# Optimization experiments

Measured on AMD Instinct MI355X. Metric: run time of the kernel, lower is better.

The kernel has to match this reference:

```python
import jax, jax.numpy as jnp
import numpy as np
from itertools import permutations

NEG = -1e30  # finite 'log-zero' sentinel to keep grads NaN-free
DEN_SCALE = 1.0


def fsm_log_marginal(llh, seqlen, src, dst, pdf, weight, init, final):
    """Log-marginal (total log path weight) of an FSM over a sequence.

    llh: [T, C] frame pdf log-likelihoods; arcs (src,dst,pdf,weight): [A];
    init/final: [N] state log-weights. Forward recursion:
      alpha_{t+1}[j] = logsumexp_{arcs a: dst=j} alpha_t[src_a] + w_a + llh[t, pdf_a]
    Frames t >= seqlen are identity (alpha frozen).
    """
    N = init.shape[0]
    T = llh.shape[0]

    def step(alpha, xs):
        llh_t, t = xs
        score = alpha[src] + weight + llh_t[pdf]  # [A]
        m = jnp.maximum(jax.ops.segment_max(score, dst, num_segments=N), NEG)
        s = jax.ops.segment_sum(jnp.exp(score - m[dst]), dst, num_segments=N)
        new = m + jnp.log(jnp.maximum(s, 1e-30))
        alpha = jnp.where(t < seqlen, new, alpha)
        return alpha, None

    alpha, _ = jax.lax.scan(step, init, (llh, jnp.arange(T)))
    return jax.nn.logsumexp(alpha + final)


# vmap over batch (FSM shared -> None axes) for the denominator
_den_b = jax.vmap(fsm_log_marginal, in_axes=(0, 0, None, None, None, None, None, None))
_den_sb = jax.vmap(_den_b, in_axes=(0, 0, None, None, None, None, None, None))
# vmap over (speaker, batch) with per-(s,b) numerator FSMs
_num_sb = jax.vmap(jax.vmap(fsm_log_marginal))


def reference(est_llhs, seqlengths, den_src, den_dst, den_pdf, den_weight,
              den_init, den_final, num_src, num_dst, num_pdf, num_weight,
              num_init, num_final):
    S = est_llhs.shape[1]
    llhs = jnp.transpose(est_llhs, (1, 0, 2, 3))  # [S, B, T, C]
    seql = seqlengths.T                           # [S, B]

    # denominator: shared graph, summed over speakers -> [B]
    den = _den_sb(llhs, seql, den_src, den_dst, den_pdf, den_weight,
                  den_init, den_final)  # [S, B]
    den_llh = den.sum(axis=0)

    # numerator: evaluate every speaker permutation, take min over perms
    num_per_perm = []
    for p in permutations(range(S)):
        pidx = jnp.array(p)
        nl = _num_sb(llhs[pidx], seql[pidx], num_src, num_dst, num_pdf,
                     num_weight, num_init, num_final)  # [S, B]
        num_per_perm.append(nl.sum(axis=0))
    num_llh = jnp.min(jnp.stack(num_per_perm, axis=1), axis=1)  # [B]

    loss = -(num_llh - DEN_SCALE * den_llh)
    return loss.sum()


def setup_inputs() -> dict:
    key = jax.random.key(0)
    ks = jax.random.split(key, 14)
    B, S, T, C = 8, 2, 512, 2048
    Nd, Ad = 1024, 16384   # denominator graph
    Nn, An = 256, 2048     # numerator graphs (per speaker, per utt)

    est_llhs = jax.nn.log_softmax(
        jax.random.normal(ks[0], (B, S, T, C), jnp.float32), axis=-1)
    seqlengths = jax.random.randint(ks[1], (B, S), T // 2, T + 1, jnp.int32)

    den_src = jax.random.randint(ks[2], (Ad,), 0, Nd, jnp.int32)
    den_dst = jax.random.randint(ks[3], (Ad,), 0, Nd, jnp.int32)
    den_pdf = jax.random.randint(ks[4], (Ad,), 0, C, jnp.int32)
    den_weight = 0.1 * jax.random.normal(ks[5], (Ad,), jnp.float32)
    den_init = jax.nn.log_softmax(jax.random.normal(ks[6], (Nd,), jnp.float32))
    den_final = jax.nn.log_softmax(jax.random.normal(ks[7], (Nd,), jnp.float32))

    num_src = jax.random.randint(ks[8], (S, B, An), 0, Nn, jnp.int32)
    num_dst = jax.random.randint(ks[9], (S, B, An), 0, Nn, jnp.int32)
    num_pdf = jax.random.randint(ks[10], (S, B, An), 0, C, jnp.int32)
    num_weight = 0.1 * jax.random.normal(ks[11], (S, B, An), jnp.float32)
    num_init = jax.nn.log_softmax(
        jax.random.normal(ks[12], (S, B, Nn), jnp.float32), axis=-1)
    num_final = jax.nn.log_softmax(
        jax.random.normal(ks[13], (S, B, Nn), jnp.float32), axis=-1)

    return {
        'est_llhs': est_llhs, 'seqlengths': seqlengths,
        'den_src': den_src, 'den_dst': den_dst, 'den_pdf': den_pdf,
        'den_weight': den_weight, 'den_init': den_init, 'den_final': den_final,
        'num_src': num_src, 'num_dst': num_dst, 'num_pdf': num_pdf,
        'num_weight': num_weight, 'num_init': num_init, 'num_final': num_final,
    }
```

## Files before the change

kernel.cpp:

```cpp
#include <hip/hip_runtime.h>
#include <cstdint>
#include <cstddef>

#define BB 8
#define SS 2
#define TT 512
#define CC 2048
#define ND 1024
#define AD 16384
#define NN 256
#define AN 2048
#define NEGV -1e30f
#define NTH 1024
#define NWG 256

__global__ void prep_kernel(const int* __restrict__ src, const int* __restrict__ dst,
                            const int* __restrict__ pdf, const float* __restrict__ w,
                            unsigned* __restrict__ meta_t, unsigned* __restrict__ pxi,
                            float* __restrict__ wcsr,
                            int* __restrict__ pbeg, int* __restrict__ padj,
                            int N, int A, int LC)
{
    __shared__ int cnt[1024];
    __shared__ int pos[1024];
    __shared__ unsigned char gcnt[8192];
    const int g = blockIdx.x;
    src += (size_t)g * A; dst += (size_t)g * A; pdf += (size_t)g * A; w += (size_t)g * A;
    meta_t += (size_t)g * A; pxi += (size_t)g * A; wcsr += (size_t)g * A;
    pbeg += (size_t)g * (N + 1); padj += (size_t)g * N;
    const int tid = threadIdx.x;
    cnt[tid] = 0;
    __syncthreads();
    for (int a = tid; a < A; a += blockDim.x) atomicAdd(&cnt[dst[a]], 1);
    __syncthreads();
    const int deg = cnt[tid];
    pos[tid] = deg;
    __syncthreads();
    for (int off = 1; off < blockDim.x; off <<= 1) {
        int add = (tid >= off) ? pos[tid - off] : 0;
        __syncthreads();
        pos[tid] += add;
        __syncthreads();
    }
    const int r0 = pos[tid] - deg;
    const int np = deg ? (((r0 + deg - 1) >> LC) - (r0 >> LC) + 1) : 0;
    __syncthreads();
    pos[tid] = np;
    __syncthreads();
    for (int off = 1; off < blockDim.x; off <<= 1) {
        int add = (tid >= off) ? pos[tid - off] : 0;
        __syncthreads();
        pos[tid] += add;
        __syncthreads();
    }
    const int pexcl = pos[tid] - np;
    pbeg[tid] = pexcl;
    if (tid == blockDim.x - 1) pbeg[N] = pexcl + np;
    padj[tid] = pexcl - (r0 >> LC);
    cnt[tid] = r0;
    __syncthreads();
    for (int a = tid; a < A; a += blockDim.x) {
        const int d2 = dst[a];
        const int p = atomicAdd(&cnt[d2], 1);
        const int l = p >> LC;
        const int i = p & ((1 << LC) - 1);
        meta_t[(size_t)i * NTH + l] = (unsigned)src[a] | ((unsigned)d2 << 16);
        pxi[p] = (unsigned)pdf[a];
        wcsr[p] = w[a];
    }
    __syncthreads();
    const int CH = 1 << LC;
    const int ngrp = (NTH / 64) * CH;
    if (tid < ngrp) {
        unsigned char* cb = &gcnt[tid * 32];
        for (int b = 0; b < 32; ++b) cb[b] = 0;
        const int i = tid & (CH - 1);
        const int w2 = tid >> LC;
        for (int lane = 0; lane < 64; ++lane) {
            const size_t idx = (size_t)i * NTH + (w2 * 64 + lane);
            const unsigned mt = meta_t[idx];
            const unsigned sv = mt & 0xffffu;
            const unsigned alt = sv ^ ((sv >> 5) & 31u);
            const int b0 = (int)(sv & 31u), b1 = (int)(alt & 31u);
            unsigned gx;
            if (cb[b1] < cb[b0]) { cb[b1]++; gx = (unsigned)N + alt; }
            else                 { cb[b0]++; gx = sv; }
            meta_t[idx] = (mt & 0xffff0000u) | gx;
        }
    }
}

__device__ void wprep_part(int ub, int nb, int t0, int Tt, const float* __restrict__ est,
                           const unsigned* __restrict__ pxi_den,
                           const float* __restrict__ wcsr_den,
                           const unsigned* __restrict__ pxi_num,
                           const float* __restrict__ wcsr_num,
                           float* __restrict__ Wd, float* __restrict__ Wn,
                           float* row_s)
{
    const int tid = threadIdx.x;
    const int nden = 16 * Tt;
    const int total = nden + 32 * Tt;
    for (int u = ub; u < total; u += nb) {
        __syncthreads();
        const float* row; const unsigned* pxi; const float* wcs; float* out; int n4;
        if (u < nden) {
            const int inst = u / Tt, trel = u - inst * Tt;
            const int s = inst >> 3, b = inst & 7;
            row = est + ((size_t)(b * SS + s) * TT + (t0 + trel)) * CC;
            pxi = pxi_den; wcs = wcsr_den;
            out = Wd + ((size_t)inst * Tt + trel) * AD;
            n4 = AD >> 2;
        } else {
            const int v = u - nden;
            const int inst = v / Tt, trel = v - inst * Tt;
            const int gg = inst & 15, p = inst >> 4;
            const int s = gg >> 3, b = gg & 7;
            const int sp = p ? (1 - s) : s;
            row = est + ((size_t)(b * SS + sp) * TT + (t0 + trel)) * CC;
            pxi = pxi_num + (size_t)gg * AN; wcs = wcsr_num + (size_t)gg * AN;
            out = Wn + ((size_t)inst * Tt + trel) * AN;
            n4 = AN >> 2;
        }
        row_s[tid] = row[tid]; row_s[tid + 1024] = row[tid + 1024];
        __syncthreads();
        const uint4* p4 = (const uint4*)pxi;
        const float4* w4 = (const float4*)wcs;
        float4* o4 = (float4*)out;
        for (int k = tid; k < n4; k += 1024) {
            const uint4 pp = p4[k];
            const float4 ww = w4[k];
            o4[k] = make_float4(row_s[pp.x] + ww.x, row_s[pp.y] + ww.y,
                                row_s[pp.z] + ww.z, row_s[pp.w] + ww.w);
        }
    }
}

__global__ __launch_bounds__(1024) void wprep0_kernel(
    const float* __restrict__ est,
    const unsigned* __restrict__ pxi_den, const float* __restrict__ wcsr_den,
    const unsigned* __restrict__ pxi_num, const float* __restrict__ wcsr_num,
    float* __restrict__ Wd, float* __restrict__ Wn, int t0, int Tt)
{
    __shared__ float row_s[CC];
    wprep_part(blockIdx.x, gridDim.x, t0, Tt, est, pxi_den, wcsr_den,
               pxi_num, wcsr_num, Wd, Wn, row_s);
}

template<int CH>
__device__ inline void load_w_row(const float* __restrict__ p, float* dst)
{
    if constexpr (CH == 16) {
        const float4* p4 = (const float4*)p;
        const float4 a = p4[0], b = p4[1], c = p4[2], d = p4[3];
        dst[0]=a.x;  dst[1]=a.y;  dst[2]=a.z;  dst[3]=a.w;
        dst[4]=b.x;  dst[5]=b.y;  dst[6]=b.z;  dst[7]=b.w;
        dst[8]=c.x;  dst[9]=c.y;  dst[10]=c.z; dst[11]=c.w;
        dst[12]=d.x; dst[13]=d.y; dst[14]=d.z; dst[15]=d.w;
    } else {
        const float2 v = *(const float2*)p;
        dst[0] = v.x; dst[1] = v.y;
    }
}

template<int CH>
__device__ void fsm_forward_tile(int N, int L, int t0, int Tt, bool first, bool last,
    const float* __restrict__ Wrow0, int wstride,
    const unsigned* __restrict__ meta_g,
    const int* __restrict__ pbeg_g, const int* __restrict__ padj_g,
    const float* __restrict__ initv, const float* __restrict__ finalv,
    float* __restrict__ alpha_gl, float* __restrict__ res,
    float* alpha_s, float2* pk)
{
    const int tid = threadIdx.x;
    unsigned meta[CH];
#pragma unroll
    for (int i = 0; i < CH; ++i) meta[i] = meta_g[i * NTH + tid];
    unsigned segmask = 0;
#pragma unroll
    for (int i = 0; i < CH; ++i) {
        const int di = (int)(meta[i] >> 16);
        const int dn = (i + 1 < CH) ? (int)(meta[i + 1] >> 16) : -1;
        if (di != dn) segmask |= (1u << i);
    }
    const int slot0 = padj_g[meta[0] >> 16] + tid;
    const bool st = tid < N;
    int pb0 = 0, pb1 = 0; float fin = 0.f;
    if (st) {
        const float a0 = first ? initv[tid] : alpha_gl[tid];
        alpha_s[tid] = a0;
        alpha_s[N + (tid ^ ((tid >> 5) & 31))] = a0;
        pb0 = pbeg_g[tid]; pb1 = pbeg_g[tid + 1];
        fin = finalv[tid];
    }
    int tb = L - t0; if (tb > Tt) tb = Tt; if (tb < 0) tb = 0;
    float wc[CH];
    if (tb > 0) load_w_row<CH>(Wrow0 + (size_t)tid * CH, wc);
    __syncthreads();

    for (int trel = 0; trel < tb; ++trel) {
        const bool pre = (trel + 1 < tb);
        float wn[CH];
        if (pre)
            load_w_row<CH>(Wrow0 + (size_t)(trel + 1) * wstride + (size_t)tid * CH, wn);
        float av[CH];
#pragma unroll
        for (int i = 0; i < CH; ++i)
            av[i] = alpha_s[meta[i] & 0xffffu];
        float sc[CH];
#pragma unroll
        for (int i = 0; i < CH; ++i)
            sc[i] = av[i] + wc[i];
        float pm[CH];
        {
            float m = -INFINITY;
#pragma unroll
            for (int i = 0; i < CH; ++i) {
                m = fmaxf(m, sc[i]);
                pm[i] = m;
                if (segmask & (1u << i)) m = -INFINITY;
            }
        }
        float sm[CH];
        sm[CH - 1] = pm[CH - 1];
#pragma unroll
        for (int i = CH - 2; i >= 0; --i)
            sm[i] = (segmask & (1u << i)) ? pm[i] : sm[i + 1];
        {
            float ssn = 0.f;
            int sl = slot0;
#pragma unroll
            for (int i = 0; i < CH; ++i) {
                ssn += __expf(sc[i] - sm[i]);
                if (segmask & (1u << i)) {
                    pk[sl] = make_float2(sm[i], ssn); ++sl;
                    ssn = 0.f;
                }
            }
        }
        __syncthreads();
        if (st) {
            float v2;
            const int cnt = pb1 - pb0;
            if (cnt > 0) {
                const float2 P0 = pk[pb0];
                const float2 P1 = pk[cnt > 1 ? pb0 + 1 : pb0];
                const float2 P2 = pk[cnt > 2 ? pb0 + 2 : pb0];
                const float2 P3 = pk[cnt > 3 ? pb0 + 3 : pb0];
                float mm = P0.x, s2 = P0.y;
                if (cnt > 1) {
                    const float d = P1.x - mm; const float e = __expf(-fabsf(d));
                    if (d > 0.f) { s2 = s2 * e + P1.y; mm = P1.x; } else { s2 += P1.y * e; }
                }
                if (cnt > 2) {
                    const float d = P2.x - mm; const float e = __expf(-fabsf(d));
                    if (d > 0.f) { s2 = s2 * e + P2.y; mm = P2.x; } else { s2 += P2.y * e; }
                }
                if (cnt > 3) {
                    const float d = P3.x - mm; const float e = __expf(-fabsf(d));
                    if (d > 0.f) { s2 = s2 * e + P3.y; mm = P3.x; } else { s2 += P3.y * e; }
                }
                for (int q2 = pb0 + 4; q2 < pb1; ++q2) {
                    const float2 Pq = pk[q2];
                    const float d = Pq.x - mm; const float e = __expf(-fabsf(d));
                    if (d > 0.f) { s2 = s2 * e + Pq.y; mm = Pq.x; } else { s2 += Pq.y * e; }
                }
                const float mc  = fmaxf(mm, NEGV);
                const float scs = s2 * __expf(mm - mc);
                v2 = mc + __logf(fmaxf(scs, 1e-30f));
            } else {
                v2 = NEGV + __logf(1e-30f);
            }
            alpha_s[tid] = v2;
            alpha_s[N + (tid ^ ((tid >> 5) & 31))] = v2;
        }
        __syncthreads();
        if (pre) {
#pragma unroll
            for (int i = 0; i < CH; ++i) wc[i] = wn[i];
        }
    }

    if (last) {
        const float v = st ? (alpha_s[tid] + fin) : -INFINITY;
        float* red = (float*)pk;
        red[tid] = v;
        __syncthreads();
        for (int off = 512; off > 0; off >>= 1) {
            if (tid < off) red[tid] = fmaxf(red[tid], red[tid + off]);
            __syncthreads();
        }
        const float M = red[0];
        __syncthreads();
        red[tid] = __expf(v - M);
        __syncthreads();
        for (int off = 512; off > 0; off >>= 1) {
            if (tid < off) red[tid] += red[tid + off];
            __syncthreads();
        }
        if (tid == 0) *res = M + __logf(red[0]);
    } else if (st) {
        alpha_gl[tid] = alpha_s[tid];
    }
}

__global__ __launch_bounds__(1024) void fused_kernel(
    const int* __restrict__ seqlen,
    const float* __restrict__ Wd, const float* __restrict__ Wn,
    const unsigned* __restrict__ den_meta,
    const int* __restrict__ den_pbeg, const int* __restrict__ den_padj,
    const float* __restrict__ den_init, const float* __restrict__ den_final,
    const unsigned* __restrict__ num_meta,
    const int* __restrict__ num_pbeg, const int* __restrict__ num_padj,
    const float* __restrict__ num_init, const float* __restrict__ num_final,
    float* __restrict__ alpha_g, float* __restrict__ res,
    int t0, int Tt, int last,
    const float* __restrict__ est,
    const unsigned* __restrict__ pxi_den, const float* __restrict__ wcsr_den,
    const unsigned* __restrict__ pxi_num, const float* __restrict__ wcsr_num,
    float* __restrict__ Wd_next, float* __restrict__ Wn_next)
{
    __shared__ float alpha[2048];
    __shared__ float2 pk[2048];
    __shared__ float row_s[CC];
    const int bid = blockIdx.x;
    const bool first = (t0 == 0);
    if (bid >= 48) {
        if (!last)
            wprep_part(bid - 48, NWG - 48, t0 + Tt, Tt, est,
                       pxi_den, wcsr_den, pxi_num, wcsr_num,
                       Wd_next, Wn_next, row_s);
        return;
    }
    if (bid < 16) {
        const int s = bid >> 3, b = bid & 7;
        const int L = seqlen[b * SS + s];
        fsm_forward_tile<16>(ND, L, t0, Tt, first, last != 0,
                             Wd + (size_t)bid * Tt * AD, AD,
                             den_meta, den_pbeg, den_padj,
                             den_init, den_final,
                             alpha_g + (size_t)bid * 1024, &res[bid], alpha, pk);
    } else {
        const int q = bid - 16;
        const int p = q >> 4, g = q & 15;
        const int s = g >> 3, b = g & 7;
        const int sp = p ? (1 - s) : s;
        const int L = seqlen[b * SS + sp];
        fsm_forward_tile<2>(NN, L, t0, Tt, first, last != 0,
                            Wn + (size_t)q * Tt * AN, AN,
                            num_meta + (size_t)g * AN,
                            num_pbeg + (size_t)g * (NN + 1), num_padj + (size_t)g * NN,
                            num_init + (size_t)g * NN, num_final + (size_t)g * NN,
                            alpha_g + (size_t)bid * 1024, &res[16 + q], alpha, pk);
    }
}

__global__ void finalize_kernel(const float* __restrict__ res, float* __restrict__ out)
{
    if (threadIdx.x == 0 && blockIdx.x == 0) {
        float loss = 0.f;
        for (int b = 0; b < BB; ++b) {
            const float den = res[b] + res[8 + b];
            const float n0  = res[16 + b] + res[16 + 8 + b];
            const float n1  = res[32 + b] + res[32 + 8 + b];
            const float nm  = fminf(n0, n1);
            loss += -(nm - den);
        }
        out[0] = loss;
    }
}

extern "C" void kernel_launch(void* const* d_in, const int* in_sizes, int n_in,
                              void* d_out, int out_size, void* d_ws, size_t ws_size,
                              hipStream_t stream)
{
    const float* est       = (const float*)d_in[0];
    const int*   seqlen    = (const int*)  d_in[1];
    const int*   den_src   = (const int*)  d_in[2];
    const int*   den_dst   = (const int*)  d_in[3];
    const int*   den_pdf   = (const int*)  d_in[4];
    const float* den_w     = (const float*)d_in[5];
    const float* den_init  = (const float*)d_in[6];
    const float* den_final = (const float*)d_in[7];
    const int*   num_src   = (const int*)  d_in[8];
    const int*   num_dst   = (const int*)  d_in[9];
    const int*   num_pdf   = (const int*)  d_in[10];
    const float* num_w     = (const float*)d_in[11];
    const float* num_init  = (const float*)d_in[12];
    const float* num_final = (const float*)d_in[13];

    char* ws = (char*)d_ws;
    unsigned* den_meta = (unsigned*)(ws + 0);
    unsigned* den_pxi  = (unsigned*)(ws + 65536);
    float*    den_wcsr = (float*)   (ws + 131072);
    unsigned* num_meta = (unsigned*)(ws + 196608);
    unsigned* num_pxi  = (unsigned*)(ws + 327680);
    float*    num_wcsr = (float*)   (ws + 458752);
    int*      num_pbeg = (int*)     (ws + 589824);
    int*      num_padj = (int*)     (ws + 606272);
    int*      den_pbeg = (int*)     (ws + 622656);
    int*      den_padj = (int*)     (ws + 626816);
    float*    alpha_g  = (float*)   (ws + 630912);
    float*    res      = (float*)   (ws + 827520);
    const size_t fixed = 827904;

    int Tt = 64;
    while (Tt > 4 && fixed + 2ull * (size_t)Tt * 1310720ull > ws_size) Tt >>= 1;
    const size_t wbuf_f = (size_t)Tt * (16 * AD + 32 * AN);
    float* Wd0 = (float*)(ws + fixed);
    float* Wn0 = Wd0 + (size_t)16 * Tt * AD;
    float* Wd1 = Wd0 + wbuf_f;
    float* Wn1 = Wd1 + (size_t)16 * Tt * AD;

    prep_kernel<<<1, 1024, 0, stream>>>(den_src, den_dst, den_pdf, den_w,
                                        den_meta, den_pxi, den_wcsr,
                                        den_pbeg, den_padj, ND, AD, 4);
    prep_kernel<<<16, 256, 0, stream>>>(num_src, num_dst, num_pdf, num_w,
                                        num_meta, num_pxi, num_wcsr,
                                        num_pbeg, num_padj, NN, AN, 1);

    wprep0_kernel<<<256, 1024, 0, stream>>>(est, den_pxi, den_wcsr,
                                            num_pxi, num_wcsr, Wd0, Wn0, 0, Tt);

    const int nt = TT / Tt;
    for (int k = 0; k < nt; ++k) {
        float* WdC = (k & 1) ? Wd1 : Wd0;
        float* WnC = (k & 1) ? Wn1 : Wn0;
        float* WdN = (k & 1) ? Wd0 : Wd1;
        float* WnN = (k & 1) ? Wn0 : Wn1;
        fused_kernel<<<NWG, 1024, 0, stream>>>(seqlen, WdC, WnC,
                                               den_meta, den_pbeg, den_padj,
                                               den_init, den_final,
                                               num_meta, num_pbeg, num_padj,
                                               num_init, num_final,
                                               alpha_g, res, k * Tt, Tt,
                                               (k == nt - 1) ? 1 : 0,
                                               est, den_pxi, den_wcsr,
                                               num_pxi, num_wcsr, WdN, WnN);
    }

    finalize_kernel<<<1, 64, 0, stream>>>(res, (float*)d_out);
}
```

Baseline: 1.275 ms.

## Replace per-tile kernel launches with a persistent cooperative kernel using grid sync

Merges the weight-prep launch, the per-tile fused launches and the finalize launch into one cooperative persistent kernel. Blocks 0-47 run the forward recursions, keep alpha in shared memory across tiles and use grid.sync between tiles. The remaining blocks prepare the next tile's weights. This removes kernel-launch gaps and the global alpha save/restore between tiles. In exchange it adds grid-wide barriers and depends on cooperative launch, falling back to the old multi-launch path if that launch fails.

```diff
diff --git a/kernel.cpp b/kernel.cpp
--- a/kernel.cpp
+++ b/kernel.cpp
@@ -1,6 +1,9 @@
 #include <hip/hip_runtime.h>
+#include <hip/hip_cooperative_groups.h>
 #include <cstdint>
 #include <cstddef>
+
+namespace cg = cooperative_groups;
 
 #define BB 8
 #define SS 2
@@ -164,6 +167,86 @@
 }
 
 template<int CH>
+__device__ inline void fsm_step(const unsigned* meta, unsigned segmask, int slot0,
+                                bool st, int pb0, int pb1, int N,
+                                const float* wc, float* alpha_s, float2* pk)
+{
+    const int tid = threadIdx.x;
+    float av[CH];
+#pragma unroll
+    for (int i = 0; i < CH; ++i)
+        av[i] = alpha_s[meta[i] & 0xffffu];
+    float sc[CH];
+#pragma unroll
+    for (int i = 0; i < CH; ++i)
+        sc[i] = av[i] + wc[i];
+    float pm[CH];
+    {
+        float m = -INFINITY;
+#pragma unroll
+        for (int i = 0; i < CH; ++i) {
+            m = fmaxf(m, sc[i]);
+            pm[i] = m;
+            if (segmask & (1u << i)) m = -INFINITY;
+        }
+    }
+    float sm[CH];
+    sm[CH - 1] = pm[CH - 1];
+#pragma unroll
+    for (int i = CH - 2; i >= 0; --i)
+        sm[i] = (segmask & (1u << i)) ? pm[i] : sm[i + 1];
+    {
+        float ssn = 0.f;
+        int sl = slot0;
+#pragma unroll
+        for (int i = 0; i < CH; ++i) {
+            ssn += __expf(sc[i] - sm[i]);
+            if (segmask & (1u << i)) {
+                pk[sl] = make_float2(sm[i], ssn); ++sl;
+                ssn = 0.f;
+            }
+        }
+    }
+    __syncthreads();
+    if (st) {
+        float v2;
+        const int cnt = pb1 - pb0;
+        if (cnt > 0) {
+            const float2 P0 = pk[pb0];
+            const float2 P1 = pk[cnt > 1 ? pb0 + 1 : pb0];
+            const float2 P2 = pk[cnt > 2 ? pb0 + 2 : pb0];
+            const float2 P3 = pk[cnt > 3 ? pb0 + 3 : pb0];
+            float mm = P0.x, s2 = P0.y;
+            if (cnt > 1) {
+                const float d = P1.x - mm; const float e = __expf(-fabsf(d));
+                if (d > 0.f) { s2 = s2 * e + P1.y; mm = P1.x; } else { s2 += P1.y * e; }
+            }
+            if (cnt > 2) {
+                const float d = P2.x - mm; const float e = __expf(-fabsf(d));
+                if (d > 0.f) { s2 = s2 * e + P2.y; mm = P2.x; } else { s2 += P2.y * e; }
+            }
+            if (cnt > 3) {
+                const float d = P3.x - mm; const float e = __expf(-fabsf(d));
+                if (d > 0.f) { s2 = s2 * e + P3.y; mm = P3.x; } else { s2 += P3.y * e; }
+            }
+            for (int q2 = pb0 + 4; q2 < pb1; ++q2) {
+                const float2 Pq = pk[q2];
+                const float d = Pq.x - mm; const float e = __expf(-fabsf(d));
+                if (d > 0.f) { s2 = s2 * e + Pq.y; mm = Pq.x; } else { s2 += Pq.y * e; }
+            }
+            const float mc  = fmaxf(mm, NEGV);
+            const float scs = s2 * __expf(mm - mc);
+            v2 = mc + __logf(fmaxf(scs, 1e-30f));
+        } else {
+            v2 = NEGV + __logf(1e-30f);
+        }
+        alpha_s[tid] = v2;
+        alpha_s[N + (tid ^ ((tid >> 5) & 31))] = v2;
+    }
+    __syncthreads();
+}
+
+template<int CH>
 __device__ void fsm_forward_tile(int N, int L, int t0, int Tt, bool first, bool last,
     const float* __restrict__ Wrow0, int wstride,
     const unsigned* __restrict__ meta_g,
@@ -203,78 +286,7 @@
         float wn[CH];
         if (pre)
             load_w_row<CH>(Wrow0 + (size_t)(trel + 1) * wstride + (size_t)tid * CH, wn);
-        float av[CH];
-#pragma unroll
-        for (int i = 0; i < CH; ++i)
-            av[i] = alpha_s[meta[i] & 0xffffu];
-        float sc[CH];
-#pragma unroll
-        for (int i = 0; i < CH; ++i)
-            sc[i] = av[i] + wc[i];
-        float pm[CH];
-        {
-            float m = -INFINITY;
-#pragma unroll
-            for (int i = 0; i < CH; ++i) {
-                m = fmaxf(m, sc[i]);
-                pm[i] = m;
-                if (segmask & (1u << i)) m = -INFINITY;
-            }
-        }
-        float sm[CH];
-        sm[CH - 1] = pm[CH - 1];
-#pragma unroll
-        for (int i = CH - 2; i >= 0; --i)
-            sm[i] = (segmask & (1u << i)) ? pm[i] : sm[i + 1];
-        {
-            float ssn = 0.f;
-            int sl = slot0;
-#pragma unroll
-            for (int i = 0; i < CH; ++i) {
-                ssn += __expf(sc[i] - sm[i]);
-                if (segmask & (1u << i)) {
-                    pk[sl] = make_float2(sm[i], ssn); ++sl;
-                    ssn = 0.f;
-                }
-            }
-        }
-        __syncthreads();
-        if (st) {
-            float v2;
-            const int cnt = pb1 - pb0;
-            if (cnt > 0) {
-                const float2 P0 = pk[pb0];
-                const float2 P1 = pk[cnt > 1 ? pb0 + 1 : pb0];
-                const float2 P2 = pk[cnt > 2 ? pb0 + 2 : pb0];
-                const float2 P3 = pk[cnt > 3 ? pb0 + 3 : pb0];
-                float mm = P0.x, s2 = P0.y;
-                if (cnt > 1) {
-                    const float d = P1.x - mm; const float e = __expf(-fabsf(d));
-                    if (d > 0.f) { s2 = s2 * e + P1.y; mm = P1.x; } else { s2 += P1.y * e; }
-                }
-                if (cnt > 2) {
-                    const float d = P2.x - mm; const float e = __expf(-fabsf(d));
-                    if (d > 0.f) { s2 = s2 * e + P2.y; mm = P2.x; } else { s2 += P2.y * e; }
-                }
-                if (cnt > 3) {
-                    const float d = P3.x - mm; const float e = __expf(-fabsf(d));
-                    if (d > 0.f) { s2 = s2 * e + P3.y; mm = P3.x; } else { s2 += P3.y * e; }
-                }
-                for (int q2 = pb0 + 4; q2 < pb1; ++q2) {
-                    const float2 Pq = pk[q2];
-                    const float d = Pq.x - mm; const float e = __expf(-fabsf(d));
-                    if (d > 0.f) { s2 = s2 * e + Pq.y; mm = Pq.x; } else { s2 += Pq.y * e; }
-                }
-                const float mc  = fmaxf(mm, NEGV);
-                const float scs = s2 * __expf(mm - mc);
-                v2 = mc + __logf(fmaxf(scs, 1e-30f));
-            } else {
-                v2 = NEGV + __logf(1e-30f);
-            }
-            alpha_s[tid] = v2;
-            alpha_s[N + (tid ^ ((tid >> 5) & 31))] = v2;
-        }
-        __syncthreads();
+        fsm_step<CH>(meta, segmask, slot0, st, pb0, pb1, N, wc, alpha_s, pk);
         if (pre) {
 #pragma unroll
             for (int i = 0; i < CH; ++i) wc[i] = wn[i];
@@ -301,6 +313,151 @@
         if (tid == 0) *res = M + __logf(red[0]);
     } else if (st) {
         alpha_gl[tid] = alpha_s[tid];
+    }
+}
+
+template<int CH>
+__device__ void fsm_forward_persist(cg::grid_group grid,
+    int N, int L, int nt, int Tt,
+    const float* __restrict__ W0, const float* __restrict__ W1, int wstride,
+    const unsigned* __restrict__ meta_g,
+    const int* __restrict__ pbeg_g, const int* __restrict__ padj_g,
+    const float* __restrict__ initv, const float* __restrict__ finalv,
+    float* __restrict__ res, float* alpha_s, float2* pk)
+{
+    const int tid = threadIdx.x;
+    unsigned meta[CH];
+#pragma unroll
+    for (int i = 0; i < CH; ++i) meta[i] = meta_g[i * NTH + tid];
+    unsigned segmask = 0;
+#pragma unroll
+    for (int i = 0; i < CH; ++i) {
+        const int di = (int)(meta[i] >> 16);
+        const int dn = (i + 1 < CH) ? (int)(meta[i + 1] >> 16) : -1;
+        if (di != dn) segmask |= (1u << i);
+    }
+    const int slot0 = padj_g[meta[0] >> 16] + tid;
+    const bool st = tid < N;
+    int pb0 = 0, pb1 = 0; float fin = 0.f;
+    if (st) {
+        const float a0 = initv[tid];
+        alpha_s[tid] = a0;
+        alpha_s[N + (tid ^ ((tid >> 5) & 31))] = a0;
+        pb0 = pbeg_g[tid]; pb1 = pbeg_g[tid + 1];
+        fin = finalv[tid];
+    }
+    __syncthreads();
+
+    for (int k = 0; k < nt; ++k) {
+        const float* __restrict__ Wrow0 = (k & 1) ? W1 : W0;
+        const int t0 = k * Tt;
+        int tb = L - t0; if (tb > Tt) tb = Tt; if (tb < 0) tb = 0;
+        float wc[CH];
+        if (tb > 0) load_w_row<CH>(Wrow0 + (size_t)tid * CH, wc);
+        for (int trel = 0; trel < tb; ++trel) {
+            const bool pre = (trel + 1 < tb);
+            float wn[CH];
+            if (pre)
+                load_w_row<CH>(Wrow0 + (size_t)(trel + 1) * wstride + (size_t)tid * CH, wn);
+            fsm_step<CH>(meta, segmask, slot0, st, pb0, pb1, N, wc, alpha_s, pk);
+            if (pre) {
+#pragma unroll
+                for (int i = 0; i < CH; ++i) wc[i] = wn[i];
+            }
+        }
+        if (k + 1 < nt) grid.sync();
+    }
+
+    const float v = st ? (alpha_s[tid] + fin) : -INFINITY;
+    float* red = (float*)pk;
+    red[tid] = v;
+    __syncthreads();
+    for (int off = 512; off > 0; off >>= 1) {
+        if (tid < off) red[tid] = fmaxf(red[tid], red[tid + off]);
+        __syncthreads();
+    }
+    const float M = red[0];
+    __syncthreads();
+    red[tid] = __expf(v - M);
+    __syncthreads();
+    for (int off = 512; off > 0; off >>= 1) {
+        if (tid < off) red[tid] += red[tid + off];
+        __syncthreads();
+    }
+    if (tid == 0) *res = M + __logf(red[0]);
+}
+
+__global__ __launch_bounds__(1024) void persist_kernel(
+    const int* __restrict__ seqlen,
+    float* __restrict__ Wd0, float* __restrict__ Wn0,
+    float* __restrict__ Wd1, float* __restrict__ Wn1,
+    const unsigned* __restrict__ den_meta,
+    const int* __restrict__ den_pbeg, const int* __restrict__ den_padj,
+    const float* __restrict__ den_init, const float* __restrict__ den_final,
+    const unsigned* __restrict__ num_meta,
+    const int* __restrict__ num_pbeg, const int* __restrict__ num_padj,
+    const float* __restrict__ num_init, const float* __restrict__ num_final,
+    float* __restrict__ res, int nt, int Tt,
+    const float* __restrict__ est,
+    const unsigned* __restrict__ pxi_den, const float* __restrict__ wcsr_den,
+    const unsigned* __restrict__ pxi_num, const float* __restrict__ wcsr_num,
+    float* __restrict__ out)
+{
+    __shared__ float alpha[2048];
+    __shared__ float2 pk[2048];
+    __shared__ float row_s[CC];
+    cg::grid_group grid = cg::this_grid();
+    const int bid = blockIdx.x;
+    const int tid = threadIdx.x;
+
+    wprep_part(bid, NWG, 0, Tt, est, pxi_den, wcsr_den, pxi_num, wcsr_num,
+               Wd0, Wn0, row_s);
+    __threadfence();
+    grid.sync();
+
+    if (bid < 16) {
+        const int s = bid >> 3, b = bid & 7;
+        const int L = seqlen[b * SS + s];
+        fsm_forward_persist<16>(grid, ND, L, nt, Tt,
+                                Wd0 + (size_t)bid * Tt * AD,
+                                Wd1 + (size_t)bid * Tt * AD, AD,
+                                den_meta, den_pbeg, den_padj,
+                                den_init, den_final, &res[bid], alpha, pk);
+    } else if (bid < 48) {
+        const int q = bid - 16;
+        const int p = q >> 4, g = q & 15;
+        const int s = g >> 3, b = g & 7;
+        const int sp = p ? (1 - s) : s;
+        const int L = seqlen[b * SS + sp];
+        fsm_forward_persist<2>(grid, NN, L, nt, Tt,
+                               Wn0 + (size_t)q * Tt * AN,
+                               Wn1 + (size_t)q * Tt * AN, AN,
+                               num_meta + (size_t)g * AN,
+                               num_pbeg + (size_t)g * (NN + 1),
+                               num_padj + (size_t)g * NN,
+                               num_init + (size_t)g * NN, num_final + (size_t)g * NN,
+                               &res[16 + q], alpha, pk);
+    } else {
+        for (int k = 0; k + 1 < nt; ++k) {
+            float* WdN = ((k + 1) & 1) ? Wd1 : Wd0;
+            float* WnN = ((k + 1) & 1) ? Wn1 : Wn0;
+            wprep_part(bid - 48, NWG - 48, (k + 1) * Tt, Tt, est,
+                       pxi_den, wcsr_den, pxi_num, wcsr_num, WdN, WnN, row_s);
+            __threadfence();
+            grid.sync();
+        }
+    }
+    __threadfence();
+    grid.sync();
+    if (bid == 0 && tid == 0) {
+        float loss = 0.f;
+        for (int b = 0; b < BB; ++b) {
+            const float den = res[b] + res[8 + b];
+            const float n0  = res[16 + b] + res[16 + 8 + b];
+            const float n1  = res[32 + b] + res[32 + 8 + b];
+            loss += -(fminf(n0, n1) - den);
+        }
+        out[0] = loss;
     }
 }
 
@@ -404,14 +561,6 @@
     float*    res      = (float*)   (ws + 827520);
     const size_t fixed = 827904;
 
-    int Tt = 64;
-    while (Tt > 4 && fixed + 2ull * (size_t)Tt * 1310720ull > ws_size) Tt >>= 1;
-    const size_t wbuf_f = (size_t)Tt * (16 * AD + 32 * AN);
-    float* Wd0 = (float*)(ws + fixed);
-    float* Wn0 = Wd0 + (size_t)16 * Tt * AD;
-    float* Wd1 = Wd0 + wbuf_f;
-    float* Wn1 = Wd1 + (size_t)16 * Tt * AD;
-
     prep_kernel<<<1, 1024, 0, stream>>>(den_src, den_dst, den_pdf, den_w,
                                         den_meta, den_pxi, den_wcsr,
                                         den_pbeg, den_padj, ND, AD, 4);
@@ -419,25 +568,49 @@
                                         num_meta, num_pxi, num_wcsr,
                                         num_pbeg, num_padj, NN, AN, 1);
 
-    wprep0_kernel<<<256, 1024, 0, stream>>>(est, den_pxi, den_wcsr,
-                                            num_pxi, num_wcsr, Wd0, Wn0, 0, Tt);
-
+    int Tt = 64;
+    while (Tt > 4 && fixed + 2ull * (size_t)Tt * 1310720ull > ws_size) Tt >>= 1;
     const int nt = TT / Tt;
-    for (int k = 0; k < nt; ++k) {
-        float* WdC = (k & 1) ? Wd1 : Wd0;
-        float* WnC = (k & 1) ? Wn1 : Wn0;
-        float* WdN = (k & 1) ? Wd0 : Wd1;
-        float* WnN = (k & 1) ? Wn0 : Wn1;
-        fused_kernel<<<NWG, 1024, 0, stream>>>(seqlen, WdC, WnC,
-                                               den_meta, den_pbeg, den_padj,
-                                               den_init, den_final,
-                                               num_meta, num_pbeg, num_padj,
-                                               num_init, num_final,
-                                               alpha_g, res, k * Tt, Tt,
-                                               (k == nt - 1) ? 1 : 0,
-                                               est, den_pxi, den_wcsr,
-                                               num_pxi, num_wcsr, WdN, WnN);
-    }
-
-    finalize_kernel<<<1, 64, 0, stream>>>(res, (float*)d_out);
-}
+    const size_t wbuf_f = (size_t)Tt * (16 * AD + 32 * AN);
+    float* Wd0 = (float*)(ws + fixed);
+    float* Wn0 = Wd0 + (size_t)16 * Tt * AD;
+    float* Wd1 = Wd0 + wbuf_f;
+    float* Wn1 = Wd1 + (size_t)16 * Tt * AD;
+    float* outp = (float*)d_out;
+
+    int nt_v = nt, Tt_v = Tt;
+    void* kargs[] = {
+        (void*)&seqlen, (void*)&Wd0, (void*)&Wn0, (void*)&Wd1, (void*)&Wn1,
+        (void*)&den_meta, (void*)&den_pbeg, (void*)&den_padj,
+        (void*)&den_init, (void*)&den_final,
+        (void*)&num_meta, (void*)&num_pbeg, (void*)&num_padj,
+        (void*)&num_init, (void*)&num_final,
+        (void*)&res, (void*)&nt_v, (void*)&Tt_v,
+        (void*)&est, (void*)&den_pxi, (void*)&den_wcsr,
+        (void*)&num_pxi, (void*)&num_wcsr, (void*)&outp
+    };
+    hipError_t rc = hipLaunchCooperativeKernel(
+        reinterpret_cast<const void*>(&persist_kernel),
+        dim3(NWG), dim3(1024), kargs, 0, stream);
+
+    if (rc != hipSuccess) {
+        wprep0_kernel<<<256, 1024, 0, stream>>>(est, den_pxi, den_wcsr,
+                                                num_pxi, num_wcsr, Wd0, Wn0, 0, Tt);
+        for (int k = 0; k < nt; ++k) {
+            float* WdC = (k & 1) ? Wd1 : Wd0;
+            float* WnC = (k & 1) ? Wn1 : Wn0;
+            float* WdN = (k & 1) ? Wd0 : Wd1;
+            float* WnN = (k & 1) ? Wn0 : Wn1;
+            fused_kernel<<<NWG, 1024, 0, stream>>>(seqlen, WdC, WnC,
+                                                   den_meta, den_pbeg, den_padj,
+                                                   den_init, den_final,
+                                                   num_meta, num_pbeg, num_padj,
+                                                   num_init, num_final,
+                                                   alpha_g, res, k * Tt, Tt,
+                                                   (k == nt - 1) ? 1 : 0,
+                                                   est, den_pxi, den_wcsr,
+                                                   num_pxi, num_wcsr, WdN, WnN);
+        }
+        finalize_kernel<<<1, 64, 0, stream>>>(res, outp);
+    }
+}
```

Result: slower. 2.302 ms (+80.6%).
